# Performance work log

Measured on AMD Instinct MI355X. Metric: run time of the kernel, lower is better.

Reference implementation:

```python
import jax, jax.numpy as jnp
import numpy as np

B, N, NFEAT, NHID1, NHID2 = 64, 1024, 512, 1024, 512


def setup_inputs() -> dict:
    key = jax.random.key(0)
    ks = jax.random.split(key, 9)
    stdv1 = 1.0 / np.sqrt(NHID1)
    stdv2 = 1.0 / np.sqrt(NHID2)
    stdvl = 1.0 / np.sqrt(NHID2)
    return {
        "x": jax.random.normal(ks[0], (B, N, NFEAT), dtype=jnp.float32),
        "adj": jax.random.uniform(ks[1], (B, N, N), dtype=jnp.float32),
        "length": jax.random.randint(ks[2], (B,), 1, N + 1, dtype=jnp.int32),
        "W1": jax.random.uniform(ks[3], (NFEAT, NHID1), jnp.float32, -stdv1, stdv1),
        "b1": jax.random.uniform(ks[4], (NHID1,), jnp.float32, -stdv1, stdv1),
        "W2": jax.random.uniform(ks[5], (NHID1, NHID2), jnp.float32, -stdv2, stdv2),
        "b2": jax.random.uniform(ks[6], (NHID2,), jnp.float32, -stdv2, stdv2),
        "Wl": jax.random.uniform(ks[7], (NHID2, 1), jnp.float32, -stdvl, stdvl),
        "bl": jax.random.uniform(ks[8], (1,), jnp.float32, -stdvl, stdvl),
    }


def _gc(x, adj, W, b):
    # support = x @ W per graph; output = adj @ support + b  (GraphConvolution)
    support = jnp.einsum("bnf,fh->bnh", x, W)
    return jnp.einsum("bnm,bmh->bnh", adj, support) + b


def reference(x, adj, length, W1, b1, W2, b2, Wl, bl):
    h = jax.nn.relu(_gc(x, adj, W1, b1))
    # dropout is identity in eval mode
    h = jax.nn.relu(_gc(h, adj, W2, b2))
    # ave_pooling: mean over first length[i] nodes
    mask = (jnp.arange(N)[None, :] < length[:, None]).astype(h.dtype)  # [B,N]
    pooled = jnp.einsum("bnh,bn->bh", h, mask) / length.astype(h.dtype)[:, None]
    return pooled @ Wl + bl  # [B,1]
```

## Files before the change

### kernel.cpp

```cpp
#include <hip/hip_runtime.h>
#include <hip/hip_bf16.h>
#include <stdint.h>


typedef short bf16x8 __attribute__((ext_vector_type(8)));
typedef short s16x4 __attribute__((ext_vector_type(4)));
typedef float f32x4 __attribute__((ext_vector_type(4)));

__device__ __forceinline__ unsigned short f2bf(float f) {
    union { float f; unsigned u; } v; v.f = f;
    unsigned r = v.u + 0x7fffu + ((v.u >> 16) & 1u);
    return (unsigned short)(r >> 16);
}
__device__ __forceinline__ float bf2f(unsigned short h) {
    union { unsigned u; float f; } v; v.u = ((unsigned)h) << 16;
    return v.f;
}

typedef const __attribute__((address_space(1))) void* gp1_t;
typedef __attribute__((address_space(3))) void* lp3_t;

__device__ __forceinline__ void ldsload16(const void* g, void* l) {
    __builtin_amdgcn_global_load_lds((gp1_t)(uintptr_t)g,
                                     (lp3_t)(unsigned)(uintptr_t)l,
                                     16, 0, 0);
}

#define BARF()   do { __builtin_amdgcn_s_barrier(); asm volatile("" ::: "memory"); } while (0)
#define LGKM0()  asm volatile("s_waitcnt lgkmcnt(0)" ::: "memory")
#define VMCNT4() asm volatile("s_waitcnt vmcnt(4)" ::: "memory")
#define MFMA16(d, a, b) d = __builtin_amdgcn_mfma_f32_16x16x32_bf16(a, b, d, 0, 0, 0)

template<bool BIASRELU, bool SPLIT>
__global__ __launch_bounds__(512, 1)
void gemm_nt8(const short* __restrict__ A, const short* __restrict__ B,
              short* __restrict__ C, const float* __restrict__ bias,
              int M, int N, int K,
              long long aStride, long long bStride, long long cStride,
              long long splitStride)
{
    __shared__ short sm[2][2][256 * 64];

    const int tid  = threadIdx.x;
    const int wid  = tid >> 6;
    const int lane = tid & 63;
    const int wm   = wid >> 2;
    const int wn   = wid & 3;
    const int quad = lane >> 4;
    const int l16  = lane & 15;

    const int bM = blockIdx.y * 256;
    const int bN = blockIdx.x * 256;
    const int z  = blockIdx.z;
    A += (long long)z * aStride;
    B += (long long)z * bStride;

    const int srow = tid >> 3;
    const int scbs = ((tid & 7) * 16) ^ ((srow & 7) << 4);
    const short* Ag = A + (long long)(bM + srow) * K + (scbs >> 1);
    const short* Bg = B + (long long)(bN + srow) * K + (scbs >> 1);
    const long long row64  = 64LL * K;
    const long long row128 = 128LL * K;

    #define STAGE(buf, ab, h, kt) do {                                        \
        const short* g_ = (ab ? Bg : Ag) + (h ? row128 : 0) + (kt) * 64;      \
        char* l_ = (char*)&sm[buf][ab][0] + (h) * 16384 + wid * 1024;         \
        ldsload16(g_, l_);                                                    \
        ldsload16(g_ + row64, l_ + 8192);                                     \
    } while (0)

    const int cbs0 = (quad * 16) ^ ((l16 & 7) << 4);
    const int cbs1 = (64 + quad * 16) ^ ((l16 & 7) << 4);

    #define RDA(buf, m, kk) (*(const bf16x8*)((const char*)&sm[buf][0][0]     \
        + (wm * 128 + (m) * 16 + l16) * 128 + ((kk) ? cbs1 : cbs0)))
    #define RDB(buf, n, kk) (*(const bf16x8*)((const char*)&sm[buf][1][0]     \
        + (wn * 64 + (n) * 16 + l16) * 128 + ((kk) ? cbs1 : cbs0)))

    f32x4 acc[8][4];
#pragma unroll
    for (int m = 0; m < 8; ++m) {
#pragma unroll
        for (int n = 0; n < 4; ++n) acc[m][n] = (f32x4)0.0f;
    }

    const int NT = K >> 6;

    STAGE(0, 0, 0, 0); STAGE(0, 0, 1, 0);
    STAGE(0, 1, 0, 0); STAGE(0, 1, 1, 0);
    STAGE(1, 1, 0, 1); STAGE(1, 0, 0, 1);
    VMCNT4();
    BARF();

    #define TILE_STEP(t, buf, bufn) do {                                      \
        int tn1 = (t) + 1; if (tn1 == NT) tn1 = 0;                            \
        int tn2 = (t) + 2; if (tn2 >= NT) tn2 -= NT;                          \
        bf16x8 a0[4], a1[4], p0[2], p1[2], q0[2], q1[2];                      \
             \
        _Pragma("unroll") for (int m = 0; m < 4; ++m) {                       \
            a0[m] = RDA(buf, m, 0); a1[m] = RDA(buf, m, 1); }                 \
        _Pragma("unroll") for (int n = 0; n < 2; ++n) {                       \
            p0[n] = RDB(buf, n, 0); p1[n] = RDB(buf, n, 1); }                 \
        STAGE(bufn, 0, 1, tn1);                                               \
        BARF(); LGKM0();                                                      \
        __builtin_amdgcn_s_setprio(1);                                        \
        _Pragma("unroll") for (int m = 0; m < 4; ++m) {                       \
            _Pragma("unroll") for (int n = 0; n < 2; ++n) {                   \
                MFMA16(acc[m][n], a0[m], p0[n]);                              \
                MFMA16(acc[m][n], a1[m], p1[n]); } }                          \
        __builtin_amdgcn_s_setprio(0);                                        \
        BARF();                                                               \
                       \
        _Pragma("unroll") for (int n = 0; n < 2; ++n) {                       \
            q0[n] = RDB(buf, 2 + n, 0); q1[n] = RDB(buf, 2 + n, 1); }         \
        STAGE(bufn, 1, 1, tn1);                                               \
        BARF(); LGKM0();                                                      \
        __builtin_amdgcn_s_setprio(1);                                        \
        _Pragma("unroll") for (int m = 0; m < 4; ++m) {                       \
            _Pragma("unroll") for (int n = 0; n < 2; ++n) {                   \
                MFMA16(acc[m][2 + n], a0[m], q0[n]);                          \
                MFMA16(acc[m][2 + n], a1[m], q1[n]); } }                      \
        __builtin_amdgcn_s_setprio(0);                                        \
        BARF();                                                               \
                       \
        _Pragma("unroll") for (int m = 0; m < 4; ++m) {                       \
            a0[m] = RDA(buf, 4 + m, 0); a1[m] = RDA(buf, 4 + m, 1); }         \
        STAGE(buf, 1, 0, tn2);                                                \
        BARF(); LGKM0();                                                      \
        __builtin_amdgcn_s_setprio(1);                                        \
        _Pragma("unroll") for (int m = 0; m < 4; ++m) {                       \
            _Pragma("unroll") for (int n = 0; n < 2; ++n) {                   \
                MFMA16(acc[4 + m][2 + n], a0[m], q0[n]);                      \
                MFMA16(acc[4 + m][2 + n], a1[m], q1[n]); } }                  \
        __builtin_amdgcn_s_setprio(0);                                        \
        BARF();                                                               \
           \
        STAGE(buf, 0, 0, tn2);                                                \
        BARF();                                                               \
        __builtin_amdgcn_s_setprio(1);                                        \
        _Pragma("unroll") for (int m = 0; m < 4; ++m) {                       \
            _Pragma("unroll") for (int n = 0; n < 2; ++n) {                   \
                MFMA16(acc[4 + m][n], a0[m], p0[n]);                          \
                MFMA16(acc[4 + m][n], a1[m], p1[n]); } }                      \
        __builtin_amdgcn_s_setprio(0);                                        \
        VMCNT4();      \
        BARF();                                                               \
    } while (0)

    for (int t = 0; t < NT; t += 2) {
        TILE_STEP(t, 0, 1);
        TILE_STEP(t + 1, 1, 0);
    }

#pragma unroll
    for (int m = 0; m < 8; ++m) {
        const int row0 = bM + wm * 128 + m * 16 + quad * 4;
#pragma unroll
        for (int n = 0; n < 4; ++n) {
            const int col = bN + wn * 64 + n * 16 + l16;
            float bv = 0.0f;
            if (BIASRELU) bv = bias[col];
#pragma unroll
            for (int r = 0; r < 4; ++r) {
                float val = acc[m][n][r];
                if (BIASRELU) val = fmaxf(val + bv, 0.0f);
                long long addr;
                if (SPLIT) {
                    const int bb = col >> 10;
                    const int nn = col & 1023;
                    addr = (long long)bb * splitStride
                         + (long long)(row0 + r) * 1024 + nn;
                } else {
                    addr = (long long)z * cStride
                         + (long long)(row0 + r) * N + col;
                }
                C[addr] = (short)f2bf(val);
            }
        }
    }
    #undef TILE_STEP
    #undef STAGE
    #undef RDA
    #undef RDB
}

__global__ void cvt_f32_bf16(const float4* __restrict__ in,
                             s16x4* __restrict__ out, int n4)
{
    int i = blockIdx.x * 256 + threadIdx.x;
    if (i < n4) {
        float4 v = in[i];
        s16x4 o;
        o.x = (short)f2bf(v.x); o.y = (short)f2bf(v.y);
        o.z = (short)f2bf(v.z); o.w = (short)f2bf(v.w);
        out[i] = o;
    }
}

__global__ void transpose_cvt(const float* __restrict__ in,
                              short* __restrict__ out, int R, int C)
{
    __shared__ float tile[32][33];
    const int bc = blockIdx.x * 32;
    const int br = blockIdx.y * 32;
    const int tx = threadIdx.x & 31;
    const int ty = threadIdx.x >> 5;
#pragma unroll
    for (int i = 0; i < 32; i += 8)
        tile[ty + i][tx] = in[(long long)(br + ty + i) * C + bc + tx];
    __syncthreads();
#pragma unroll
    for (int i = 0; i < 32; i += 8)
        out[(long long)(bc + ty + i) * R + br + tx] = (short)f2bf(tile[tx][ty + i]);
}

__global__ void pool_partial(const short* __restrict__ h2,
                             const int* __restrict__ length,
                             float* __restrict__ part)
{
    const int b = blockIdx.y;
    const int chunk = blockIdx.x;
    const int t = threadIdx.x;
    const int len = length[b];
    const int r0 = chunk * 128;
    const int r1 = min(r0 + 128, len);
    const unsigned* p = (const unsigned*)(h2 + (long long)b * 1024 * 512);
    float s0 = 0.0f, s1 = 0.0f;
    for (int r = r0; r < r1; r++) {
        unsigned v = p[r * 256 + t];
        s0 += bf2f((unsigned short)(v & 0xffffu));
        s1 += bf2f((unsigned short)(v >> 16));
    }
    float2 o; o.x = s0; o.y = s1;
    ((float2*)part)[(b * 8 + chunk) * 256 + t] = o;
}

__global__ void pool_final2(const float* __restrict__ part,
                            const int* __restrict__ length,
                            const float* __restrict__ Wl,
                            const float* __restrict__ bl,
                            float* __restrict__ out)
{
    const int b = blockIdx.x;
    const int t = threadIdx.x;
    float s0 = 0.0f, s1 = 0.0f;
#pragma unroll
    for (int c = 0; c < 8; c++) {
        float2 v = ((const float2*)part)[(b * 8 + c) * 256 + t];
        s0 += v.x; s1 += v.y;
    }
    float v = s0 * Wl[2 * t] + s1 * Wl[2 * t + 1];
#pragma unroll
    for (int off = 32; off > 0; off >>= 1) v += __shfl_down(v, off);
    __shared__ float wsum[4];
    if ((t & 63) == 0) wsum[t >> 6] = v;
    __syncthreads();
    if (t == 0) {
        float s = wsum[0] + wsum[1] + wsum[2] + wsum[3];
        out[b] = s / (float)length[b] + bl[0];
    }
}

extern "C" void kernel_launch(void* const* d_in, const int* in_sizes, int n_in,
                              void* d_out, int out_size, void* d_ws, size_t ws_size,
                              hipStream_t stream)
{
    const float* x    = (const float*)d_in[0];
    const float* adj  = (const float*)d_in[1];
    const int*   len  = (const int*)d_in[2];
    const float* W1   = (const float*)d_in[3];
    const float* b1   = (const float*)d_in[4];
    const float* W2   = (const float*)d_in[5];
    const float* b2   = (const float*)d_in[6];
    const float* Wl   = (const float*)d_in[7];
    const float* bl   = (const float*)d_in[8];
    float* out = (float*)d_out;

    char* ws = (char*)d_ws;
    short* adjB  = (short*)(ws);
    short* xS2T  = (short*)(ws + 134217728LL);
    short* W1T   = (short*)(ws + 201326592LL);
    short* W2T   = (short*)(ws + 202375168LL);
    short* S1Th2 = (short*)(ws + 203423744LL);
    short* h1    = (short*)(ws + 337641472LL);
    float* part  = (float*)(ws + 134217728LL + 33554432LL);

    cvt_f32_bf16<<<65536, 256, 0, stream>>>((const float4*)adj, (s16x4*)adjB, 16777216);
    cvt_f32_bf16<<<32768, 256, 0, stream>>>((const float4*)x,   (s16x4*)xS2T,  8388608);
    transpose_cvt<<<dim3(32, 16), 256, 0, stream>>>(W1, W1T, 512, 1024);
    transpose_cvt<<<dim3(16, 32), 256, 0, stream>>>(W2, W2T, 1024, 512);

    gemm_nt8<false, true><<<dim3(256, 4, 1), 512, 0, stream>>>(
        W1T, xS2T, S1Th2, nullptr, 1024, 65536, 512, 0, 0, 0, 1048576LL);

    gemm_nt8<true, false><<<dim3(4, 4, 64), 512, 0, stream>>>(
        adjB, S1Th2, h1, b1, 1024, 1024, 1024, 1048576LL, 1048576LL, 1048576LL, 0);

    gemm_nt8<false, true><<<dim3(256, 2, 1), 512, 0, stream>>>(
        W2T, h1, xS2T, nullptr, 512, 65536, 1024, 0, 0, 0, 524288LL);

    gemm_nt8<true, false><<<dim3(2, 4, 64), 512, 0, stream>>>(
        adjB, xS2T, S1Th2, b2, 1024, 512, 1024, 1048576LL, 524288LL, 524288LL, 0);

    pool_partial<<<dim3(8, 64), 256, 0, stream>>>(S1Th2, len, part);
    pool_final2<<<64, 256, 0, stream>>>(part, len, Wl, bl, out);
}
```

Baseline: 900.9 us.

## Fuse masked mean pooling into last GEMM epilogue and skip rows beyond length

The final adjacency GEMM now reduces its bias+ReLU output per column over valid rows and writes partial sums directly, so the h2 store and the separate pool_partial kernel go away. Row blocks starting past the graph length exit early, skipping GEMM work the pooling never reads. It also adds an XCD-aware block swizzle for the batched adj GEMMs and merges the two f32-to-bf16 conversion launches into one. The pooled sum now comes from fp32 accumulators rather than bf16-rounded h2, which changes numerics slightly.

```diff
diff --git a/kernel.cpp b/kernel.cpp
--- a/kernel.cpp
+++ b/kernel.cpp
@@ -29,17 +29,45 @@
 #define BARF()   do { __builtin_amdgcn_s_barrier(); asm volatile("" ::: "memory"); } while (0)
 #define LGKM0()  asm volatile("s_waitcnt lgkmcnt(0)" ::: "memory")
 #define VMCNT4() asm volatile("s_waitcnt vmcnt(4)" ::: "memory")
+#define VMCNT0() asm volatile("s_waitcnt vmcnt(0)" ::: "memory")
 #define MFMA16(d, a, b) d = __builtin_amdgcn_mfma_f32_16x16x32_bf16(a, b, d, 0, 0, 0)
 
-template<bool BIASRELU, bool SPLIT>
+template<bool BIASRELU, bool SPLIT, bool ZSWZ, bool POOL>
 __global__ __launch_bounds__(512, 1)
 void gemm_nt8(const short* __restrict__ A, const short* __restrict__ B,
               short* __restrict__ C, const float* __restrict__ bias,
               int M, int N, int K,
               long long aStride, long long bStride, long long cStride,
-              long long splitStride)
+              long long splitStride,
+              const int* __restrict__ length, float* __restrict__ pool_out)
 {
     __shared__ short sm[2][2][256 * 64];
+
+    int bx, by, bz;
+    if (ZSWZ) {
+        const int P = gridDim.x * gridDim.y;
+        const int f = blockIdx.x + gridDim.x * (blockIdx.y + gridDim.y * blockIdx.z);
+        const int k = f & 7;
+        const int j = f >> 3;
+        const int zper = gridDim.z >> 3;
+        const int jp = j / P;
+        bz = k * zper + jp;
+        const int rem = j - jp * P;
+        bx = rem % gridDim.x;
+        by = rem / gridDim.x;
+    } else {
+        bx = blockIdx.x; by = blockIdx.y; bz = blockIdx.z;
+    }
+
+    const int bM = by * 256;
+    const int bN = bx * 256;
+    const int z  = bz;
+
+    int len = 0;
+    if (POOL) {
+        len = length[z];
+        if (bM >= len) return;
+    }
 
     const int tid  = threadIdx.x;
     const int wid  = tid >> 6;
@@ -49,9 +77,6 @@
     const int quad = lane >> 4;
     const int l16  = lane & 15;
 
-    const int bM = blockIdx.y * 256;
-    const int bN = blockIdx.x * 256;
-    const int z  = blockIdx.z;
     A += (long long)z * aStride;
     B += (long long)z * bStride;
 
@@ -150,6 +175,36 @@
     for (int t = 0; t < NT; t += 2) {
         TILE_STEP(t, 0, 1);
         TILE_STEP(t + 1, 1, 0);
+    }
+
+    if (POOL) {
+        VMCNT0();
+        __syncthreads();
+        float* red = (float*)&sm[0][0][0];
+#pragma unroll
+        for (int n = 0; n < 4; ++n) {
+            const int col = wn * 64 + n * 16 + l16;
+            const float bv = bias[bN + col];
+            float cs = 0.0f;
+#pragma unroll
+            for (int m = 0; m < 8; ++m) {
+                const int row0 = bM + wm * 128 + m * 16 + quad * 4;
+#pragma unroll
+                for (int r = 0; r < 4; ++r) {
+                    const float val = fmaxf(acc[m][n][r] + bv, 0.0f);
+                    if (row0 + r < len) cs += val;
+                }
+            }
+            cs += __shfl_xor(cs, 16);
+            cs += __shfl_xor(cs, 32);
+            if (quad == 0) red[wm * 256 + col] = cs;
+        }
+        __syncthreads();
+        if (tid < 256) {
+            const float s = red[tid] + red[256 + tid];
+            pool_out[((long long)z * 4 + by) * 512 + bN + tid] = s;
+        }
+        return;
     }
 
 #pragma unroll
@@ -184,17 +239,18 @@
     #undef RDB
 }
 
-__global__ void cvt_f32_bf16(const float4* __restrict__ in,
-                             s16x4* __restrict__ out, int n4)
+__global__ void cvt2_f32_bf16(const float4* __restrict__ inA, s16x4* __restrict__ outA, int nA4,
+                              const float4* __restrict__ inB, s16x4* __restrict__ outB, int nB4)
 {
     int i = blockIdx.x * 256 + threadIdx.x;
-    if (i < n4) {
-        float4 v = in[i];
-        s16x4 o;
-        o.x = (short)f2bf(v.x); o.y = (short)f2bf(v.y);
-        o.z = (short)f2bf(v.z); o.w = (short)f2bf(v.w);
-        out[i] = o;
-    }
+    const float4* in; s16x4* out; int j;
+    if (i < nA4) { in = inA; out = outA; j = i; }
+    else { j = i - nA4; if (j >= nB4) return; in = inB; out = outB; }
+    float4 v = in[j];
+    s16x4 o;
+    o.x = (short)f2bf(v.x); o.y = (short)f2bf(v.y);
+    o.z = (short)f2bf(v.z); o.w = (short)f2bf(v.w);
+    out[j] = o;
 }
 
 __global__ void transpose_cvt(const float* __restrict__ in,
@@ -214,28 +270,7 @@
         out[(long long)(bc + ty + i) * R + br + tx] = (short)f2bf(tile[tx][ty + i]);
 }
 
-__global__ void pool_partial(const short* __restrict__ h2,
-                             const int* __restrict__ length,
-                             float* __restrict__ part)
-{
-    const int b = blockIdx.y;
-    const int chunk = blockIdx.x;
-    const int t = threadIdx.x;
-    const int len = length[b];
-    const int r0 = chunk * 128;
-    const int r1 = min(r0 + 128, len);
-    const unsigned* p = (const unsigned*)(h2 + (long long)b * 1024 * 512);
-    float s0 = 0.0f, s1 = 0.0f;
-    for (int r = r0; r < r1; r++) {
-        unsigned v = p[r * 256 + t];
-        s0 += bf2f((unsigned short)(v & 0xffffu));
-        s1 += bf2f((unsigned short)(v >> 16));
-    }
-    float2 o; o.x = s0; o.y = s1;
-    ((float2*)part)[(b * 8 + chunk) * 256 + t] = o;
-}
-
-__global__ void pool_final2(const float* __restrict__ part,
+__global__ void pool_final3(const float* __restrict__ part,
                             const int* __restrict__ length,
                             const float* __restrict__ Wl,
                             const float* __restrict__ bl,
@@ -243,10 +278,11 @@
 {
     const int b = blockIdx.x;
     const int t = threadIdx.x;
+    const int len = length[b];
+    const int mbmax = (len + 255) >> 8;
     float s0 = 0.0f, s1 = 0.0f;
-#pragma unroll
-    for (int c = 0; c < 8; c++) {
-        float2 v = ((const float2*)part)[(b * 8 + c) * 256 + t];
+    for (int mb = 0; mb < mbmax; mb++) {
+        float2 v = ((const float2*)part)[(b * 4 + mb) * 256 + t];
         s0 += v.x; s1 += v.y;
     }
     float v = s0 * Wl[2 * t] + s1 * Wl[2 * t + 1];
@@ -257,7 +293,7 @@
     __syncthreads();
     if (t == 0) {
         float s = wsum[0] + wsum[1] + wsum[2] + wsum[3];
-        out[b] = s / (float)length[b] + bl[0];
+        out[b] = s / (float)len + bl[0];
     }
 }
 
@@ -281,27 +317,27 @@
     short* xS2T  = (short*)(ws + 134217728LL);
     short* W1T   = (short*)(ws + 201326592LL);
     short* W2T   = (short*)(ws + 202375168LL);
-    short* S1Th2 = (short*)(ws + 203423744LL);
+    short* S1T   = (short*)(ws + 203423744LL);
     short* h1    = (short*)(ws + 337641472LL);
     float* part  = (float*)(ws + 134217728LL + 33554432LL);
 
-    cvt_f32_bf16<<<65536, 256, 0, stream>>>((const float4*)adj, (s16x4*)adjB, 16777216);
-    cvt_f32_bf16<<<32768, 256, 0, stream>>>((const float4*)x,   (s16x4*)xS2T,  8388608);
+    cvt2_f32_bf16<<<98304, 256, 0, stream>>>(
+        (const float4*)adj, (s16x4*)adjB, 16777216,
+        (const float4*)x,   (s16x4*)xS2T,  8388608);
     transpose_cvt<<<dim3(32, 16), 256, 0, stream>>>(W1, W1T, 512, 1024);
     transpose_cvt<<<dim3(16, 32), 256, 0, stream>>>(W2, W2T, 1024, 512);
 
-    gemm_nt8<false, true><<<dim3(256, 4, 1), 512, 0, stream>>>(
-        W1T, xS2T, S1Th2, nullptr, 1024, 65536, 512, 0, 0, 0, 1048576LL);
-
-    gemm_nt8<true, false><<<dim3(4, 4, 64), 512, 0, stream>>>(
-        adjB, S1Th2, h1, b1, 1024, 1024, 1024, 1048576LL, 1048576LL, 1048576LL, 0);
-
-    gemm_nt8<false, true><<<dim3(256, 2, 1), 512, 0, stream>>>(
-        W2T, h1, xS2T, nullptr, 512, 65536, 1024, 0, 0, 0, 524288LL);
-
-    gemm_nt8<true, false><<<dim3(2, 4, 64), 512, 0, stream>>>(
-        adjB, xS2T, S1Th2, b2, 1024, 512, 1024, 1048576LL, 524288LL, 524288LL, 0);
-
-    pool_partial<<<dim3(8, 64), 256, 0, stream>>>(S1Th2, len, part);
-    pool_final2<<<64, 256, 0, stream>>>(part, len, Wl, bl, out);
-}
+    gemm_nt8<false, true, false, false><<<dim3(256, 4, 1), 512, 0, stream>>>(
+        W1T, xS2T, S1T, nullptr, 1024, 65536, 512, 0, 0, 0, 1048576LL, nullptr, nullptr);
+
+    gemm_nt8<true, false, true, false><<<dim3(4, 4, 64), 512, 0, stream>>>(
+        adjB, S1T, h1, b1, 1024, 1024, 1024, 1048576LL, 1048576LL, 1048576LL, 0, nullptr, nullptr);
+
+    gemm_nt8<false, true, false, false><<<dim3(256, 2, 1), 512, 0, stream>>>(
+        W2T, h1, xS2T, nullptr, 512, 65536, 1024, 0, 0, 0, 524288LL, nullptr, nullptr);
+
+    gemm_nt8<true, false, true, true><<<dim3(2, 4, 64), 512, 0, stream>>>(
+        adjB, xS2T, nullptr, b2, 1024, 512, 1024, 1048576LL, 524288LL, 0, 0, len, part);
+
+    pool_final3<<<64, 256, 0, stream>>>(part, len, Wl, bl, out);
+}
```

Result: faster. 808.5 us (-10.3%).
